# Kernel optimization log

Hardware: AMD Instinct MI355X
Metric: run time of the kernel (lower is better)

## Reference

```python
import jax, jax.numpy as jnp
import numpy as np

NEG_SLOPE = 0.2

def setup_inputs() -> dict:
    key = jax.random.key(0)
    k1, k2, k3, k4 = jax.random.split(key, 4)
    N, K, C_IN, C_OUT = 8192, 4, 512, 512
    inputs = jax.random.normal(k1, (N, C_IN), dtype=jnp.float32)
    adj_set = jax.random.uniform(k2, (K, N, N), dtype=jnp.float32)
    att = jax.random.uniform(k3, (K,), dtype=jnp.float32)
    # xavier_uniform for w
    limit = float(np.sqrt(6.0 / (C_IN + C_OUT)))
    w = jax.random.uniform(k4, (C_IN, C_OUT), minval=-limit, maxval=limit, dtype=jnp.float32)
    b = jnp.zeros((C_OUT,), dtype=jnp.float32)
    return {"inputs": inputs, "adj_set": adj_set, "att": att, "w": w, "b": b}

def reference(inputs, adj_set, att, w, b):
    # support: [N, C_out]
    support = inputs @ w + b
    # residual=True path: outputs = sum_i att[i] * (adj_i @ support)
    #                             = (sum_i att[i] * adj_i) @ support
    combined_adj = jnp.einsum('k,knm->nm', att, adj_set)  # [N, N]
    outputs = combined_adj @ support                       # [N, C_out]
    # LeakyReLU(negative_slope=0.2)
    return jnp.where(outputs >= 0, outputs, NEG_SLOPE * outputs)
```

## Files before the change

### kernel.cpp

```cpp
#include <hip/hip_runtime.h>

#define LP 40

typedef __attribute__((ext_vector_type(8))) short short8;
typedef __attribute__((ext_vector_type(4))) short short4t;
typedef __attribute__((ext_vector_type(4))) float f32x4;

__device__ __forceinline__ short f2bf(float f) {
  unsigned u = __builtin_bit_cast(unsigned, f);
  u += 0x7FFFu + ((u >> 16) & 1u);
  return (short)(u >> 16);
}

__device__ __forceinline__ float lrelu(float v) { return v >= 0.f ? v : 0.2f * v; }

__global__ __launch_bounds__(256) void k_wt(const float* __restrict__ w,
                                            short* __restrict__ wt) {
  __shared__ float t[64][65];
  int c0 = (blockIdx.x & 7) * 64;
  int n0 = (blockIdx.x >> 3) * 64;
  int r  = threadIdx.x >> 4;
  int q4 = (threadIdx.x & 15) * 4;
  for (int i = 0; i < 4; i++) {
    int c = r + i * 16;
    f32x4 v = *(const f32x4*)(w + (size_t)(c0 + c) * 512 + (n0 + q4));
    t[c][q4 + 0] = v[0]; t[c][q4 + 1] = v[1]; t[c][q4 + 2] = v[2]; t[c][q4 + 3] = v[3];
  }
  __syncthreads();
  for (int i = 0; i < 4; i++) {
    int n = r + i * 16;
    short4t o;
    for (int j = 0; j < 4; j++) o[j] = f2bf(t[q4 + j][n]);
    *(short4t*)(wt + (size_t)(n0 + n) * 512 + (c0 + q4)) = o;
  }
}

__global__ __launch_bounds__(512, 2) void k_support(const float* __restrict__ inp,
                                                    const short* __restrict__ wt,
                                                    const float* __restrict__ bias,
                                                    short* __restrict__ sup) {
  __shared__ __align__(16) short As[512 * LP];
  __shared__ __align__(16) short Bs[64 * LP];
  const int tid = threadIdx.x;
  const int m0 = blockIdx.x * 64;
  const int wave = tid >> 6, lane = tid & 63;
  const int wn = wave >> 1, wm = wave & 1;
  const int lr = lane & 15, lk = lane >> 4;
  const int bm = tid >> 3, bk = (tid & 7) * 4;
  f32x4 acc[8][2] = {};
  short8 ar[4]; f32x4 br;
  auto loadA = [&](int s) {
    const short* p = wt + (size_t)tid * 512 + s * 32;
    ar[0] = *(const short8*)(p);      ar[1] = *(const short8*)(p + 8);
    ar[2] = *(const short8*)(p + 16); ar[3] = *(const short8*)(p + 24);
  };
  auto loadB = [&](int s) {
    br = *(const f32x4*)(inp + (size_t)(m0 + bm) * 512 + s * 32 + bk);
  };
  loadA(0); loadB(0);
  for (int s = 0; s < 16; s++) {
    short* ad = As + tid * LP;
    *(short8*)(ad) = ar[0]; *(short8*)(ad + 8) = ar[1];
    *(short8*)(ad + 16) = ar[2]; *(short8*)(ad + 24) = ar[3];
    short4t bo;
    for (int j = 0; j < 4; j++) bo[j] = f2bf(br[j]);
    *(short4t*)(Bs + bm * LP + bk) = bo;
    __syncthreads();
    if (s + 1 < 16) { loadA(s + 1); loadB(s + 1); }
    short8 af[8], bfr[2];
    for (int nf = 0; nf < 8; nf++)
      af[nf] = *(const short8*)(As + (wn * 128 + nf * 16 + lr) * LP + lk * 8);
    for (int mf = 0; mf < 2; mf++)
      bfr[mf] = *(const short8*)(Bs + (wm * 32 + mf * 16 + lr) * LP + lk * 8);
    for (int nf = 0; nf < 8; nf++)
      for (int mf = 0; mf < 2; mf++)
        acc[nf][mf] = __builtin_amdgcn_mfma_f32_16x16x32_bf16(af[nf], bfr[mf], acc[nf][mf], 0, 0, 0);
    __syncthreads();
  }
  for (int nf = 0; nf < 8; nf++) {
    int nb = wn * 128 + nf * 16 + lk * 4;
    for (int mf = 0; mf < 2; mf++) {
      int m = m0 + wm * 32 + mf * 16 + lr;
      for (int j = 0; j < 4; j++) {
        int n = nb + j;
        sup[(size_t)n * 8192 + m] = f2bf(acc[nf][mf][j] + bias[n]);
      }
    }
  }
}

__global__ __launch_bounds__(512, 2) void k_main(const float* __restrict__ adj,
                                                 const float* __restrict__ att,
                                                 const short* __restrict__ sup,
                                                 float* __restrict__ part,
                                                 float* __restrict__ outp,
                                                 int ksplit) {
  __shared__ __align__(16) short As[512 * LP];
  __shared__ __align__(16) short Bs[64 * LP];
  const int tid = threadIdx.x;
  const int m0 = blockIdx.x * 64;
  const int kc = blockIdx.y;
  const int kchunk = 8192 / ksplit;
  const int nsteps = kchunk / 32;
  const int kbase = kc * kchunk;
  const float t0 = att[0], t1 = att[1], t2 = att[2], t3 = att[3];
  const int wave = tid >> 6, lane = tid & 63;
  const int wn = wave >> 1, wm = wave & 1;
  const int lr = lane & 15, lk = lane >> 4;
  const int bm = tid >> 3, bk = (tid & 7) * 4;
  f32x4 acc[8][2] = {};
  const float* adjp = adj + (size_t)(m0 + bm) * 8192 + kbase + bk;
  short8 ar[4]; f32x4 br[4];
  auto loadA = [&](int s) {
    const short* p = sup + (size_t)tid * 8192 + kbase + s * 32;
    ar[0] = *(const short8*)(p);      ar[1] = *(const short8*)(p + 8);
    ar[2] = *(const short8*)(p + 16); ar[3] = *(const short8*)(p + 24);
  };
  auto loadB = [&](int s) {
    const float* q = adjp + (size_t)s * 32;
    br[0] = *(const f32x4*)(q);
    br[1] = *(const f32x4*)(q + (1ull << 26));
    br[2] = *(const f32x4*)(q + (2ull << 26));
    br[3] = *(const f32x4*)(q + (3ull << 26));
  };
  loadA(0); loadB(0);
  for (int s = 0; s < nsteps; s++) {
    short* ad = As + tid * LP;
    *(short8*)(ad) = ar[0]; *(short8*)(ad + 8) = ar[1];
    *(short8*)(ad + 16) = ar[2]; *(short8*)(ad + 24) = ar[3];
    short4t bo;
    for (int j = 0; j < 4; j++)
      bo[j] = f2bf(t0 * br[0][j] + t1 * br[1][j] + t2 * br[2][j] + t3 * br[3][j]);
    *(short4t*)(Bs + bm * LP + bk) = bo;
    __syncthreads();
    if (s + 1 < nsteps) { loadA(s + 1); loadB(s + 1); }
    short8 af[8], bfr[2];
    for (int nf = 0; nf < 8; nf++)
      af[nf] = *(const short8*)(As + (wn * 128 + nf * 16 + lr) * LP + lk * 8);
    for (int mf = 0; mf < 2; mf++)
      bfr[mf] = *(const short8*)(Bs + (wm * 32 + mf * 16 + lr) * LP + lk * 8);
    for (int nf = 0; nf < 8; nf++)
      for (int mf = 0; mf < 2; mf++)
        acc[nf][mf] = __builtin_amdgcn_mfma_f32_16x16x32_bf16(af[nf], bfr[mf], acc[nf][mf], 0, 0, 0);
    __syncthreads();
  }
  for (int nf = 0; nf < 8; nf++) {
    int n = wn * 128 + nf * 16 + lk * 4;
    for (int mf = 0; mf < 2; mf++) {
      int m = m0 + wm * 32 + mf * 16 + lr;
      f32x4 v = acc[nf][mf];
      if (ksplit == 1) {
        for (int j = 0; j < 4; j++) v[j] = lrelu(v[j]);
        *(f32x4*)(outp + (size_t)m * 512 + n) = v;
      } else {
        *(f32x4*)(part + (size_t)kc * (8192 * 512) + (size_t)m * 512 + n) = v;
      }
    }
  }
}

__global__ __launch_bounds__(256) void k_reduce(const float* __restrict__ part,
                                                float* __restrict__ outp) {
  const size_t total = (size_t)8192 * 512 / 4;
  for (size_t i = (size_t)blockIdx.x * 256 + threadIdx.x; i < total;
       i += (size_t)gridDim.x * 256) {
    f32x4 a = *(const f32x4*)(part + i * 4);
    f32x4 b = *(const f32x4*)(part + (size_t)8192 * 512 + i * 4);
    f32x4 v;
    for (int j = 0; j < 4; j++) v[j] = lrelu(a[j] + b[j]);
    *(f32x4*)(outp + i * 4) = v;
  }
}

extern "C" void kernel_launch(void* const* d_in, const int* in_sizes, int n_in,
                              void* d_out, int out_size, void* d_ws, size_t ws_size,
                              hipStream_t stream) {
  const float* inputs = (const float*)d_in[0];
  const float* adj    = (const float*)d_in[1];
  const float* att    = (const float*)d_in[2];
  const float* w      = (const float*)d_in[3];
  const float* bias   = (const float*)d_in[4];
  float* outp = (float*)d_out;

  char* ws = (char*)d_ws;
  short* sup  = (short*)(ws);
  short* wt   = (short*)(ws + (8u << 20));
  float* part = (float*)(ws + (9u << 20));

  size_t need2 = (9ull << 20) + 2ull * 8192 * 512 * 4;
  int ksplit = (ws_size >= need2) ? 2 : 1;

  k_wt<<<64, 256, 0, stream>>>(w, wt);
  k_support<<<128, 512, 0, stream>>>(inputs, wt, bias, sup);
  dim3 g2(128, (unsigned)ksplit);
  k_main<<<g2, 512, 0, stream>>>(adj, att, sup, part, outp, ksplit);
  if (ksplit == 2) k_reduce<<<2048, 256, 0, stream>>>(part, outp);
}
```

Baseline: 357.8 us.

## Retile main GEMM to 128-row tiles with direct support loads and XCD-aware split-K

The main adjacency×support kernel now uses 128-row output tiles. Each wave loads its support fragments straight from global memory instead of staging them in LDS, and a double-buffered LDS tile for the combined adjacency removes one barrier per step. Split-K can now go up to 4, with blocks mapped so each XCD handles one K chunk. Adjacency reads and the output and partial stores use nontemporal hints. In exchange it adds more partial-sum traffic for the reduce pass, launches fewer blocks per K chunk, and repeats global loads of support data from every block.

```diff
diff --git a/kernel.cpp b/kernel.cpp
--- a/kernel.cpp
+++ b/kernel.cpp
@@ -95,80 +95,90 @@
                                                  float* __restrict__ part,
                                                  float* __restrict__ outp,
                                                  int ksplit) {
-  __shared__ __align__(16) short As[512 * LP];
-  __shared__ __align__(16) short Bs[64 * LP];
+  __shared__ __align__(16) short Bs[2][128 * LP];
   const int tid = threadIdx.x;
-  const int m0 = blockIdx.x * 64;
-  const int kc = blockIdx.y;
+  const int b = blockIdx.x;
+  const int xpk = 8 / ksplit;
+  const int xcd = b & 7;
+  const int kc = xcd / xpk;
+  const int m0 = ((b >> 3) * xpk + (xcd % xpk)) * 128;
   const int kchunk = 8192 / ksplit;
   const int nsteps = kchunk / 32;
   const int kbase = kc * kchunk;
   const float t0 = att[0], t1 = att[1], t2 = att[2], t3 = att[3];
   const int wave = tid >> 6, lane = tid & 63;
-  const int wn = wave >> 1, wm = wave & 1;
   const int lr = lane & 15, lk = lane >> 4;
-  const int bm = tid >> 3, bk = (tid & 7) * 4;
-  f32x4 acc[8][2] = {};
-  const float* adjp = adj + (size_t)(m0 + bm) * 8192 + kbase + bk;
-  short8 ar[4]; f32x4 br[4];
-  auto loadA = [&](int s) {
-    const short* p = sup + (size_t)tid * 8192 + kbase + s * 32;
-    ar[0] = *(const short8*)(p);      ar[1] = *(const short8*)(p + 8);
-    ar[2] = *(const short8*)(p + 16); ar[3] = *(const short8*)(p + 24);
+  const int srow = tid >> 2, koff = (tid & 3) * 8;
+  f32x4 acc[4][8] = {};
+  const float* adjp = adj + (size_t)(m0 + srow) * 8192 + kbase + koff;
+  const short* supp = sup + (size_t)(wave * 64 + lr) * 8192 + kbase + lk * 8;
+  f32x4 br[8];
+  auto loadAdj = [&](int s) {
+    const float* q = adjp + (size_t)s * 32;
+#pragma unroll
+    for (int mt = 0; mt < 4; mt++) {
+      br[mt * 2]     = __builtin_nontemporal_load((const f32x4*)(q + ((size_t)mt << 26)));
+      br[mt * 2 + 1] = __builtin_nontemporal_load((const f32x4*)(q + ((size_t)mt << 26) + 4));
+    }
   };
-  auto loadB = [&](int s) {
-    const float* q = adjp + (size_t)s * 32;
-    br[0] = *(const f32x4*)(q);
-    br[1] = *(const f32x4*)(q + (1ull << 26));
-    br[2] = *(const f32x4*)(q + (2ull << 26));
-    br[3] = *(const f32x4*)(q + (3ull << 26));
-  };
-  loadA(0); loadB(0);
+  loadAdj(0);
+  int p = 0;
   for (int s = 0; s < nsteps; s++) {
-    short* ad = As + tid * LP;
-    *(short8*)(ad) = ar[0]; *(short8*)(ad + 8) = ar[1];
-    *(short8*)(ad + 16) = ar[2]; *(short8*)(ad + 24) = ar[3];
-    short4t bo;
-    for (int j = 0; j < 4; j++)
-      bo[j] = f2bf(t0 * br[0][j] + t1 * br[1][j] + t2 * br[2][j] + t3 * br[3][j]);
-    *(short4t*)(Bs + bm * LP + bk) = bo;
+    short8 af[4];
+#pragma unroll
+    for (int nf = 0; nf < 4; nf++)
+      af[nf] = *(const short8*)(supp + (size_t)(nf * 16) * 8192 + s * 32);
+    short8 bo;
+#pragma unroll
+    for (int k2 = 0; k2 < 8; k2++) {
+      int h = k2 >> 2, j = k2 & 3;
+      float c = t0 * br[h][j] + t1 * br[2 + h][j] + t2 * br[4 + h][j] + t3 * br[6 + h][j];
+      bo[k2] = f2bf(c);
+    }
+    *(short8*)(Bs[p] + srow * LP + koff) = bo;
     __syncthreads();
-    if (s + 1 < nsteps) { loadA(s + 1); loadB(s + 1); }
-    short8 af[8], bfr[2];
-    for (int nf = 0; nf < 8; nf++)
-      af[nf] = *(const short8*)(As + (wn * 128 + nf * 16 + lr) * LP + lk * 8);
-    for (int mf = 0; mf < 2; mf++)
-      bfr[mf] = *(const short8*)(Bs + (wm * 32 + mf * 16 + lr) * LP + lk * 8);
-    for (int nf = 0; nf < 8; nf++)
-      for (int mf = 0; mf < 2; mf++)
+    if (s + 1 < nsteps) loadAdj(s + 1);
+    short8 bfr[8];
+#pragma unroll
+    for (int mf = 0; mf < 8; mf++)
+      bfr[mf] = *(const short8*)(Bs[p] + (mf * 16 + lr) * LP + lk * 8);
+#pragma unroll
+    for (int nf = 0; nf < 4; nf++)
+#pragma unroll
+      for (int mf = 0; mf < 8; mf++)
         acc[nf][mf] = __builtin_amdgcn_mfma_f32_16x16x32_bf16(af[nf], bfr[mf], acc[nf][mf], 0, 0, 0);
-    __syncthreads();
-  }
-  for (int nf = 0; nf < 8; nf++) {
-    int n = wn * 128 + nf * 16 + lk * 4;
-    for (int mf = 0; mf < 2; mf++) {
-      int m = m0 + wm * 32 + mf * 16 + lr;
+    p ^= 1;
+  }
+#pragma unroll
+  for (int nf = 0; nf < 4; nf++) {
+    int n = wave * 64 + nf * 16 + lk * 4;
+#pragma unroll
+    for (int mf = 0; mf < 8; mf++) {
+      int m = m0 + mf * 16 + lr;
       f32x4 v = acc[nf][mf];
       if (ksplit == 1) {
         for (int j = 0; j < 4; j++) v[j] = lrelu(v[j]);
-        *(f32x4*)(outp + (size_t)m * 512 + n) = v;
+        __builtin_nontemporal_store(v, (f32x4*)(outp + (size_t)m * 512 + n));
       } else {
-        *(f32x4*)(part + (size_t)kc * (8192 * 512) + (size_t)m * 512 + n) = v;
+        __builtin_nontemporal_store(v, (f32x4*)(part + ((size_t)kc << 22) + (size_t)m * 512 + n));
       }
     }
   }
 }
 
 __global__ __launch_bounds__(256) void k_reduce(const float* __restrict__ part,
-                                                float* __restrict__ outp) {
+                                                float* __restrict__ outp, int ksplit) {
   const size_t total = (size_t)8192 * 512 / 4;
   for (size_t i = (size_t)blockIdx.x * 256 + threadIdx.x; i < total;
        i += (size_t)gridDim.x * 256) {
-    f32x4 a = *(const f32x4*)(part + i * 4);
-    f32x4 b = *(const f32x4*)(part + (size_t)8192 * 512 + i * 4);
+    f32x4 a = __builtin_nontemporal_load((const f32x4*)(part + i * 4));
+    for (int k = 1; k < ksplit; k++) {
+      f32x4 bv = __builtin_nontemporal_load((const f32x4*)(part + ((size_t)k << 22) + i * 4));
+      for (int j = 0; j < 4; j++) a[j] += bv[j];
+    }
     f32x4 v;
-    for (int j = 0; j < 4; j++) v[j] = lrelu(a[j] + b[j]);
-    *(f32x4*)(outp + i * 4) = v;
+    for (int j = 0; j < 4; j++) v[j] = lrelu(a[j]);
+    __builtin_nontemporal_store(v, (f32x4*)(outp + i * 4));
   }
 }
 
@@ -187,12 +197,13 @@
   short* wt   = (short*)(ws + (8u << 20));
   float* part = (float*)(ws + (9u << 20));
 
-  size_t need2 = (9ull << 20) + 2ull * 8192 * 512 * 4;
-  int ksplit = (ws_size >= need2) ? 2 : 1;
+  const size_t base = (9ull << 20), psz = (1ull << 24);
+  int ksplit = 1;
+  if (ws_size >= base + 4 * psz) ksplit = 4;
+  else if (ws_size >= base + 2 * psz) ksplit = 2;
 
   k_wt<<<64, 256, 0, stream>>>(w, wt);
   k_support<<<128, 512, 0, stream>>>(inputs, wt, bias, sup);
-  dim3 g2(128, (unsigned)ksplit);
-  k_main<<<g2, 512, 0, stream>>>(adj, att, sup, part, outp, ksplit);
-  if (ksplit == 2) k_reduce<<<2048, 256, 0, stream>>>(part, outp);
-}
+  k_main<<<64 * ksplit, 512, 0, stream>>>(adj, att, sup, part, outp, ksplit);
+  if (ksplit > 1) k_reduce<<<1024, 256, 0, stream>>>(part, outp, ksplit);
+}
```

Result: faster. 337.3 us (-5.7%).
